# Kernel optimization log

Measured on AMD Instinct MI355X. Metric: run time of the kernel, lower is better.

## Reference

```python
import jax, jax.numpy as jnp
import numpy as np

N_SPK = 2048
M_UTT = 16
D_EMB = 512
EPS = 1e-8  # torch cosine_similarity eps


def setup_inputs() -> dict:
    key = jax.random.key(0)
    k1, = jax.random.split(key, 1)
    speaker_vectors = jax.random.normal(k1, (N_SPK * M_UTT, D_EMB), dtype=jnp.float32)
    return {
        "speaker_vectors": speaker_vectors,
        "w": jnp.float32(10.0),
        "b": jnp.float32(-5.0),
        "speakers": N_SPK,
    }


def _normalize(x):
    # torch.cosine_similarity clamps each norm at eps
    n = jnp.maximum(jnp.linalg.norm(x, axis=-1, keepdims=True), EPS)
    return x / n


def reference(speaker_vectors, w, b, speakers):
    N = speakers
    NM, D = speaker_vectors.shape
    M = NM // N
    v3 = speaker_vectors.reshape(N, M, D)
    ssum = v3.sum(axis=1)                         # [N, D] per-speaker sums
    C = ssum / M                                  # full centroids [N, D]
    C_min = (ssum[:, None, :] - v3) / (M - 1)     # leave-one-out centroids [N, M, D]

    vn = _normalize(speaker_vectors)              # [NM, D]
    # diagonal similarities: cos(C_min[j], v[j]) per utterance j
    S_diag = jnp.sum(_normalize(C_min.reshape(NM, D)) * vn, axis=-1)  # [NM]
    # full similarity matrix via one normalized matmul: [N, NM]
    S_full = _normalize(C) @ vn.T
    # replace each speaker's own block row entries with leave-one-out sims
    col_spk = jnp.arange(NM) // M                 # speaker id of each column
    same = col_spk[None, :] == jnp.arange(N)[:, None]  # [N, NM]
    S = jnp.where(same, S_diag[None, :], S_full)

    # L_j = -(w*S_diag_j + b) + log sum_n exp(w*S[n,j] + b)
    L = -(w * S_diag + b) + jax.nn.logsumexp(w * S + b, axis=0)
    return L.sum()
```

## Files before the change

### kernel.cpp

```cpp
#include <hip/hip_runtime.h>
#include <stdint.h>

#define N_SPK 2048
#define M_UTT 16
#define D_EMB 512
#define NM (N_SPK * M_UTT)
#define FP8_SCALE 16.0f

typedef __attribute__((ext_vector_type(4))) float f32x4;

__device__ __forceinline__ void async_copy16(const void* g, void* l) {
    __builtin_amdgcn_global_load_lds(
        (const __attribute__((address_space(1))) unsigned int*)g,
        (__attribute__((address_space(3))) unsigned int*)l,
        16, 0, 0);
}

__global__ __launch_bounds__(256) void prep_kernel(
    const float* __restrict__ V, const float* __restrict__ wp,
    const float* __restrict__ bp, unsigned char* __restrict__ Cn8,
    unsigned char* __restrict__ vn8, float* __restrict__ dterm,
    float* __restrict__ colsum, float* __restrict__ out)
{
    const int spk = blockIdx.x, t = threadIdx.x;
    const int wave = t >> 6, lane = t & 63;
    const float2* vb = (const float2*)(V + (size_t)spk * (M_UTT * D_EMB));

    __shared__ __align__(16) float red[32][264];
    __shared__ float red2[32];
    __shared__ float invs[M_UTT];
    __shared__ float wred[4];

    if (spk < 128) colsum[spk * 256 + t] = 0.f;
    if (spk == 0 && t == 0) out[0] = 0.f;

    float2 p[M_UTT];
#pragma unroll
    for (int m = 0; m < M_UTT; ++m) p[m] = vb[m * 256 + t];

    float2 ss = make_float2(0.f, 0.f);
#pragma unroll
    for (int m = 0; m < M_UTT; ++m) { ss.x += p[m].x; ss.y += p[m].y; }

    float cnp = ss.x * ss.x + ss.y * ss.y;
#pragma unroll
    for (int off = 32; off > 0; off >>= 1) cnp += __shfl_xor(cnp, off);
    if (lane == 0) wred[wave] = cnp;

#pragma unroll
    for (int m = 0; m < M_UTT; ++m) {
        red[m][t]         = ss.x * p[m].x + ss.y * p[m].y;
        red[m + M_UTT][t] = p[m].x * p[m].x + p[m].y * p[m].y;
    }
    __syncthreads();
    const float cn2 = wred[0] + wred[1] + wred[2] + wred[3];

    {
        const int r = t >> 3, s = t & 7;
        const float4* rp = (const float4*)red;
        float4 a = make_float4(0.f, 0.f, 0.f, 0.f);
#pragma unroll
        for (int k = 0; k < 8; ++k) {
            float4 q = rp[r * 66 + s + 8 * k];
            a.x += q.x; a.y += q.y; a.z += q.z; a.w += q.w;
        }
        float v1 = (a.x + a.y) + (a.z + a.w);
        v1 += __shfl_xor(v1, 1);
        v1 += __shfl_xor(v1, 2);
        v1 += __shfl_xor(v1, 4);
        if (s == 0) red2[r] = v1;
    }
    __syncthreads();

    if (t < M_UTT) {
        const float sv = red2[t], vv = red2[t + M_UTT];
        const float cc = cn2 - 2.f * sv + vv;
        const float cv = sv - vv;
        const float dc = fmaxf(sqrtf(fmaxf(cc, 0.f)) * (1.f / (M_UTT - 1)), 1e-8f) * (M_UTT - 1);
        const float dv = fmaxf(sqrtf(vv), 1e-8f);
        dterm[spk * M_UTT + t] = (*wp) * (cv / (dc * dv)) + (*bp);
        invs[t] = FP8_SCALE / dv;
    }
    __syncthreads();

    const float cs = FP8_SCALE / (M_UTT * fmaxf(sqrtf(cn2) * (1.f / M_UTT), 1e-8f));
    {
        int pk = __builtin_amdgcn_cvt_pk_fp8_f32(ss.x * cs, ss.y * cs, 0, false);
        ((unsigned short*)(Cn8 + (size_t)spk * D_EMB))[t] = (unsigned short)pk;
    }
#pragma unroll
    for (int m = 0; m < M_UTT; ++m) {
        const float iv = invs[m];
        int pk = __builtin_amdgcn_cvt_pk_fp8_f32(p[m].x * iv, p[m].y * iv, 0, false);
        ((unsigned short*)(vn8 + ((size_t)(spk * M_UTT + m)) * D_EMB))[t] = (unsigned short)pk;
    }
}

__global__ __launch_bounds__(256) void gemm_kernel(
    const unsigned char* __restrict__ Cn8, const unsigned char* __restrict__ vn8,
    const float* __restrict__ wp, const float* __restrict__ bp,
    float* __restrict__ colsum)
{
    __shared__ __align__(16) unsigned char As[128 * 64];
    __shared__ __align__(16) unsigned char Bs[128 * 64];
    __shared__ float csum[128];

    const int tid = threadIdx.x;
    const int w = tid >> 6, l = tid & 63;
    const int by = blockIdx.x;
    const int bx = blockIdx.y;
    const float wgt = (*wp) * (1.f / (FP8_SCALE * FP8_SCALE));
    const float bsc = *bp;

    if (tid < 128) csum[tid] = 0.f;

    const int srow = w * 32 + (l >> 2);
    const int sj   = ((l & 3) ^ ((l >> 2) ^ (l >> 4))) & 3;
    const unsigned char* Ab = Cn8 + (size_t)(by * 128 + srow) * D_EMB + sj * 16;
    const unsigned char* Bb = vn8 + (size_t)(bx * 128 + srow) * D_EMB + sj * 16;
    unsigned char* AsW = As + w * 2048;
    unsigned char* BsW = Bs + w * 2048;

    const int wm = w & 1, wn = w >> 1;
    const int l16 = l & 15, q = l >> 4;
    const int sl = (l16 ^ (l16 >> 2)) & 3;
    const int off0 = (((q >> 1)    ) ^ sl) * 16 + (q & 1) * 8;
    const int off1 = (((q >> 1) + 2) ^ sl) * 16 + (q & 1) * 8;
    const unsigned char* Ard = As + (wm * 64 + l16) * 64;
    const unsigned char* Brd = Bs + (wn * 64 + l16) * 64;

    f32x4 acc[4][4];
    const f32x4 z = {0.f, 0.f, 0.f, 0.f};
#pragma unroll
    for (int i = 0; i < 4; ++i)
#pragma unroll
        for (int j = 0; j < 4; ++j) acc[i][j] = z;

    for (int kk = 0; kk < D_EMB; kk += 64) {
        __syncthreads();
        async_copy16(Ab + kk, AsW);
        async_copy16(Ab + 16 * D_EMB + kk, AsW + 1024);
        async_copy16(Bb + kk, BsW);
        async_copy16(Bb + 16 * D_EMB + kk, BsW + 1024);
        __syncthreads();
#pragma unroll
        for (int h = 0; h < 2; ++h) {
            const int off = h ? off1 : off0;
            long af[4], bfr[4];
#pragma unroll
            for (int i = 0; i < 4; ++i) af[i] = *(const long*)(Ard + i * 16 * 64 + off);
#pragma unroll
            for (int j = 0; j < 4; ++j) bfr[j] = *(const long*)(Brd + j * 16 * 64 + off);
#pragma unroll
            for (int i = 0; i < 4; ++i)
#pragma unroll
                for (int j = 0; j < 4; ++j)
                    acc[i][j] = __builtin_amdgcn_mfma_f32_16x16x32_fp8_fp8(
                        af[i], bfr[j], acc[i][j], 0, 0, 0);
        }
    }

    const int rowg0 = by * 128 + wm * 64 + q * 4;
    const int colg0 = bx * 128 + wn * 64 + l16;
#pragma unroll
    for (int j = 0; j < 4; ++j) {
        const int colg = colg0 + j * 16;
        const int cspk = colg >> 4;
        float p = 0.f;
#pragma unroll
        for (int i = 0; i < 4; ++i) {
            const int rowg = rowg0 + i * 16;
#pragma unroll
            for (int r = 0; r < 4; ++r) {
                float e = __expf(wgt * acc[i][j][r] + bsc);
                p += (rowg + r == cspk) ? 0.f : e;
            }
        }
        p += __shfl_xor(p, 16);
        p += __shfl_xor(p, 32);
        if (q == 0) atomicAdd(&csum[wn * 64 + j * 16 + l16], p);
    }
    __syncthreads();
    if (tid < 128) atomicAdd(&colsum[bx * 128 + tid], csum[tid]);
}

__global__ __launch_bounds__(256) void finish_kernel(
    const float* __restrict__ dterm, const float* __restrict__ colsum,
    float* __restrict__ out)
{
    const int idx = blockIdx.x * 256 + threadIdx.x;
    const int stride = gridDim.x * 256;
    float local = 0.f;
    for (int j = idx; j < NM; j += stride) {
        float t = dterm[j];
        local += logf(colsum[j] + __expf(t)) - t;
    }
#pragma unroll
    for (int off = 32; off > 0; off >>= 1) local += __shfl_xor(local, off);
    __shared__ float wr[4];
    const int wave = threadIdx.x >> 6, lane = threadIdx.x & 63;
    if (lane == 0) wr[wave] = local;
    __syncthreads();
    if (threadIdx.x == 0) atomicAdd(out, wr[0] + wr[1] + wr[2] + wr[3]);
}

extern "C" void kernel_launch(void* const* d_in, const int* in_sizes, int n_in,
                              void* d_out, int out_size, void* d_ws, size_t ws_size,
                              hipStream_t stream) {
    const float* V  = (const float*)d_in[0];
    const float* wp = (const float*)d_in[1];
    const float* bp = (const float*)d_in[2];

    char* ws = (char*)d_ws;
    unsigned char* Cn8 = (unsigned char*)ws;
    unsigned char* vn8 = (unsigned char*)(ws + ((size_t)1 << 20));
    float* dterm  = (float*)(ws + ((size_t)17 << 20));
    float* colsum = dterm + NM;
    float* out    = (float*)d_out;

    prep_kernel<<<N_SPK, 256, 0, stream>>>(V, wp, bp, Cn8, vn8, dterm, colsum, out);
    gemm_kernel<<<dim3(N_SPK / 128, NM / 128), 256, 0, stream>>>(Cn8, vn8, wp, bp, colsum);
    finish_kernel<<<64, 256, 0, stream>>>(dterm, colsum, out);
}
```

Before: 153.1 us.

## Use scaled 16x16x128 FP8 MFMA with 128-wide K tiles and fuse finish into GEMM

```diff
diff --git a/kernel.cpp b/kernel.cpp
--- a/kernel.cpp
+++ b/kernel.cpp
@@ -8,6 +8,8 @@
 #define FP8_SCALE 16.0f
 
 typedef __attribute__((ext_vector_type(4))) float f32x4;
+typedef __attribute__((ext_vector_type(4))) int   i32x4;
+typedef __attribute__((ext_vector_type(8))) int   i32x8;
 
 __device__ __forceinline__ void async_copy16(const void* g, void* l) {
     __builtin_amdgcn_global_load_lds(
@@ -16,11 +18,17 @@
         16, 0, 0);
 }
 
+__device__ __forceinline__ i32x8 ld_frag(const unsigned char* base, int s0) {
+    i32x4 lo = *(const i32x4*)(base + s0 * 16);
+    i32x4 hi = *(const i32x4*)(base + (s0 ^ 1) * 16);
+    return __builtin_shufflevector(lo, hi, 0, 1, 2, 3, 4, 5, 6, 7);
+}
+
 __global__ __launch_bounds__(256) void prep_kernel(
     const float* __restrict__ V, const float* __restrict__ wp,
     const float* __restrict__ bp, unsigned char* __restrict__ Cn8,
     unsigned char* __restrict__ vn8, float* __restrict__ dterm,
-    float* __restrict__ colsum, float* __restrict__ out)
+    float* __restrict__ colsum, int* __restrict__ cnt, float* __restrict__ out)
 {
     const int spk = blockIdx.x, t = threadIdx.x;
     const int wave = t >> 6, lane = t & 63;
@@ -32,6 +40,7 @@
     __shared__ float wred[4];
 
     if (spk < 128) colsum[spk * 256 + t] = 0.f;
+    if (spk == 128) cnt[t] = 0;
     if (spk == 0 && t == 0) out[0] = 0.f;
 
     float2 p[M_UTT];
@@ -99,11 +108,14 @@
 __global__ __launch_bounds__(256) void gemm_kernel(
     const unsigned char* __restrict__ Cn8, const unsigned char* __restrict__ vn8,
     const float* __restrict__ wp, const float* __restrict__ bp,
-    float* __restrict__ colsum)
+    float* __restrict__ colsum, const float* __restrict__ dterm,
+    int* __restrict__ cnt, float* __restrict__ out)
 {
-    __shared__ __align__(16) unsigned char As[128 * 64];
-    __shared__ __align__(16) unsigned char Bs[128 * 64];
+    __shared__ __align__(16) unsigned char As[128 * 128];
+    __shared__ __align__(16) unsigned char Bs[128 * 128];
     __shared__ float csum[128];
+    __shared__ float fin[2];
+    __shared__ int lastf;
 
     const int tid = threadIdx.x;
     const int w = tid >> 6, l = tid & 63;
@@ -114,20 +126,18 @@
 
     if (tid < 128) csum[tid] = 0.f;
 
-    const int srow = w * 32 + (l >> 2);
-    const int sj   = ((l & 3) ^ ((l >> 2) ^ (l >> 4))) & 3;
-    const unsigned char* Ab = Cn8 + (size_t)(by * 128 + srow) * D_EMB + sj * 16;
-    const unsigned char* Bb = vn8 + (size_t)(bx * 128 + srow) * D_EMB + sj * 16;
-    unsigned char* AsW = As + w * 2048;
-    unsigned char* BsW = Bs + w * 2048;
+    const int srow = w * 32 + (l >> 3);
+    const int sg   = (l & 7) ^ ((l >> 3) & 7);
+    const unsigned char* Ab = Cn8 + (size_t)(by * 128 + srow) * D_EMB + sg * 16;
+    const unsigned char* Bb = vn8 + (size_t)(bx * 128 + srow) * D_EMB + sg * 16;
+    unsigned char* AsW = As + (w * 32) * 128;
+    unsigned char* BsW = Bs + (w * 32) * 128;
 
     const int wm = w & 1, wn = w >> 1;
     const int l16 = l & 15, q = l >> 4;
-    const int sl = (l16 ^ (l16 >> 2)) & 3;
-    const int off0 = (((q >> 1)    ) ^ sl) * 16 + (q & 1) * 8;
-    const int off1 = (((q >> 1) + 2) ^ sl) * 16 + (q & 1) * 8;
-    const unsigned char* Ard = As + (wm * 64 + l16) * 64;
-    const unsigned char* Brd = Bs + (wn * 64 + l16) * 64;
+    const int s0 = ((l >> 3) & 6) ^ (l & 7);
+    const unsigned char* Ard = As + (wm * 64 + l16) * 128;
+    const unsigned char* Brd = Bs + (wn * 64 + l16) * 128;
 
     f32x4 acc[4][4];
     const f32x4 z = {0.f, 0.f, 0.f, 0.f};
@@ -136,27 +146,24 @@
 #pragma unroll
         for (int j = 0; j < 4; ++j) acc[i][j] = z;
 
-    for (int kk = 0; kk < D_EMB; kk += 64) {
+    for (int kk = 0; kk < D_EMB; kk += 128) {
         __syncthreads();
-        async_copy16(Ab + kk, AsW);
-        async_copy16(Ab + 16 * D_EMB + kk, AsW + 1024);
-        async_copy16(Bb + kk, BsW);
-        async_copy16(Bb + 16 * D_EMB + kk, BsW + 1024);
+#pragma unroll
+        for (int i = 0; i < 4; ++i) {
+            async_copy16(Ab + kk + (size_t)(i * 8) * D_EMB, AsW + i * 1024);
+            async_copy16(Bb + kk + (size_t)(i * 8) * D_EMB, BsW + i * 1024);
+        }
         __syncthreads();
-#pragma unroll
-        for (int h = 0; h < 2; ++h) {
-            const int off = h ? off1 : off0;
-            long af[4], bfr[4];
-#pragma unroll
-            for (int i = 0; i < 4; ++i) af[i] = *(const long*)(Ard + i * 16 * 64 + off);
-#pragma unroll
-            for (int j = 0; j < 4; ++j) bfr[j] = *(const long*)(Brd + j * 16 * 64 + off);
-#pragma unroll
-            for (int i = 0; i < 4; ++i)
-#pragma unroll
-                for (int j = 0; j < 4; ++j)
-                    acc[i][j] = __builtin_amdgcn_mfma_f32_16x16x32_fp8_fp8(
-                        af[i], bfr[j], acc[i][j], 0, 0, 0);
+        i32x8 bfr[4];
+#pragma unroll
+        for (int j = 0; j < 4; ++j) bfr[j] = ld_frag(Brd + j * 2048, s0);
+#pragma unroll
+        for (int i = 0; i < 4; ++i) {
+            i32x8 af = ld_frag(Ard + i * 2048, s0);
+#pragma unroll
+            for (int j = 0; j < 4; ++j)
+                acc[i][j] = __builtin_amdgcn_mfma_scale_f32_16x16x128_f8f6f4(
+                    af, bfr[j], acc[i][j], 0, 0, 0, 0x7F7F7F7F, 0, 0x7F7F7F7F);
         }
     }
 
@@ -182,26 +189,28 @@
     }
     __syncthreads();
     if (tid < 128) atomicAdd(&colsum[bx * 128 + tid], csum[tid]);
-}
-
-__global__ __launch_bounds__(256) void finish_kernel(
-    const float* __restrict__ dterm, const float* __restrict__ colsum,
-    float* __restrict__ out)
-{
-    const int idx = blockIdx.x * 256 + threadIdx.x;
-    const int stride = gridDim.x * 256;
-    float local = 0.f;
-    for (int j = idx; j < NM; j += stride) {
-        float t = dterm[j];
-        local += logf(colsum[j] + __expf(t)) - t;
-    }
-#pragma unroll
-    for (int off = 32; off > 0; off >>= 1) local += __shfl_xor(local, off);
-    __shared__ float wr[4];
-    const int wave = threadIdx.x >> 6, lane = threadIdx.x & 63;
-    if (lane == 0) wr[wave] = local;
-    __syncthreads();
-    if (threadIdx.x == 0) atomicAdd(out, wr[0] + wr[1] + wr[2] + wr[3]);
+    __syncthreads();
+
+    if (tid == 0) {
+        __threadfence();
+        lastf = (atomicAdd(&cnt[bx], 1) == (int)gridDim.x - 1);
+    }
+    __syncthreads();
+    if (lastf) {
+        __threadfence();
+        float loc = 0.f;
+        if (tid < 128) {
+            const int jj = bx * 128 + tid;
+            const float csv = atomicAdd(&colsum[jj], 0.0f);
+            const float dt  = dterm[jj];
+            loc = logf(csv + __expf(dt)) - dt;
+        }
+#pragma unroll
+        for (int off = 32; off > 0; off >>= 1) loc += __shfl_xor(loc, off);
+        if (l == 0 && w < 2) fin[w] = loc;
+        __syncthreads();
+        if (tid == 0) atomicAdd(out, fin[0] + fin[1]);
+    }
 }
 
 extern "C" void kernel_launch(void* const* d_in, const int* in_sizes, int n_in,
@@ -216,9 +225,10 @@
     unsigned char* vn8 = (unsigned char*)(ws + ((size_t)1 << 20));
     float* dterm  = (float*)(ws + ((size_t)17 << 20));
     float* colsum = dterm + NM;
+    int*   cnt    = (int*)(colsum + NM);
     float* out    = (float*)d_out;
 
-    prep_kernel<<<N_SPK, 256, 0, stream>>>(V, wp, bp, Cn8, vn8, dterm, colsum, out);
-    gemm_kernel<<<dim3(N_SPK / 128, NM / 128), 256, 0, stream>>>(Cn8, vn8, wp, bp, colsum);
-    finish_kernel<<<64, 256, 0, stream>>>(dterm, colsum, out);
-}
+    prep_kernel<<<N_SPK, 256, 0, stream>>>(V, wp, bp, Cn8, vn8, dterm, colsum, cnt, out);
+    gemm_kernel<<<dim3(N_SPK / 128, NM / 128), 256, 0, stream>>>(
+        Cn8, vn8, wp, bp, colsum, dterm, cnt, out);
+}
```

Result: slower. 445.1 us (+190.7%).

## Switch GEMM to 16x16x128 scaled FP8 MFMA with 256-byte K tiles

Applied to the files above, without the earlier changes.

```diff
diff --git a/kernel.cpp b/kernel.cpp
--- a/kernel.cpp
+++ b/kernel.cpp
@@ -8,12 +8,20 @@
 #define FP8_SCALE 16.0f
 
 typedef __attribute__((ext_vector_type(4))) float f32x4;
+typedef __attribute__((ext_vector_type(4))) int   i32x4;
+typedef __attribute__((ext_vector_type(8))) int   i32x8;
 
 __device__ __forceinline__ void async_copy16(const void* g, void* l) {
     __builtin_amdgcn_global_load_lds(
         (const __attribute__((address_space(1))) unsigned int*)g,
         (__attribute__((address_space(3))) unsigned int*)l,
         16, 0, 0);
+}
+
+__device__ __forceinline__ i32x8 ld_frag(const unsigned char* base, int s0) {
+    i32x4 lo = *(const i32x4*)(base + s0 * 16);
+    i32x4 hi = *(const i32x4*)(base + (s0 ^ 1) * 16);
+    return __builtin_shufflevector(lo, hi, 0, 1, 2, 3, 4, 5, 6, 7);
 }
 
 __global__ __launch_bounds__(256) void prep_kernel(
@@ -101,8 +109,8 @@
     const float* __restrict__ wp, const float* __restrict__ bp,
     float* __restrict__ colsum)
 {
-    __shared__ __align__(16) unsigned char As[128 * 64];
-    __shared__ __align__(16) unsigned char Bs[128 * 64];
+    __shared__ __align__(16) unsigned char As[128 * 256];
+    __shared__ __align__(16) unsigned char Bs[128 * 256];
     __shared__ float csum[128];
 
     const int tid = threadIdx.x;
@@ -114,20 +122,21 @@
 
     if (tid < 128) csum[tid] = 0.f;
 
-    const int srow = w * 32 + (l >> 2);
-    const int sj   = ((l & 3) ^ ((l >> 2) ^ (l >> 4))) & 3;
-    const unsigned char* Ab = Cn8 + (size_t)(by * 128 + srow) * D_EMB + sj * 16;
-    const unsigned char* Bb = vn8 + (size_t)(bx * 128 + srow) * D_EMB + sj * 16;
-    unsigned char* AsW = As + w * 2048;
-    unsigned char* BsW = Bs + w * 2048;
+    const int r_l = l >> 4, hh = (l >> 3) & 1, sl8 = l & 7;
+    const int g_even = sl8 ^ r_l;
+    const size_t rowoff = (size_t)(w * 32 + r_l) * D_EMB + hh * 128;
+    const unsigned char* Ab0 = Cn8 + (size_t)(by * 128) * D_EMB + rowoff + g_even * 16;
+    const unsigned char* Ab1 = Cn8 + (size_t)(by * 128) * D_EMB + rowoff + (g_even ^ 4) * 16;
+    const unsigned char* Bb0 = vn8 + (size_t)(bx * 128) * D_EMB + rowoff + g_even * 16;
+    const unsigned char* Bb1 = vn8 + (size_t)(bx * 128) * D_EMB + rowoff + (g_even ^ 4) * 16;
+    unsigned char* AsW = As + (w * 32) * 256;
+    unsigned char* BsW = Bs + (w * 32) * 256;
 
     const int wm = w & 1, wn = w >> 1;
     const int l16 = l & 15, q = l >> 4;
-    const int sl = (l16 ^ (l16 >> 2)) & 3;
-    const int off0 = (((q >> 1)    ) ^ sl) * 16 + (q & 1) * 8;
-    const int off1 = (((q >> 1) + 2) ^ sl) * 16 + (q & 1) * 8;
-    const unsigned char* Ard = As + (wm * 64 + l16) * 64;
-    const unsigned char* Brd = Bs + (wn * 64 + l16) * 64;
+    const int s0 = (2 * q) ^ (l & 7);
+    const unsigned char* Ard = As + (wm * 64 + l16) * 256;
+    const unsigned char* Brd = Bs + (wn * 64 + l16) * 256;
 
     f32x4 acc[4][4];
     const f32x4 z = {0.f, 0.f, 0.f, 0.f};
@@ -136,27 +145,31 @@
 #pragma unroll
         for (int j = 0; j < 4; ++j) acc[i][j] = z;
 
-    for (int kk = 0; kk < D_EMB; kk += 64) {
+#pragma unroll
+    for (int kk = 0; kk < D_EMB; kk += 256) {
         __syncthreads();
-        async_copy16(Ab + kk, AsW);
-        async_copy16(Ab + 16 * D_EMB + kk, AsW + 1024);
-        async_copy16(Bb + kk, BsW);
-        async_copy16(Bb + 16 * D_EMB + kk, BsW + 1024);
+#pragma unroll
+        for (int i = 0; i < 8; ++i) {
+            const unsigned char* pa = ((i & 1) ? Ab1 : Ab0) + i * 2048 + kk;
+            const unsigned char* pb = ((i & 1) ? Bb1 : Bb0) + i * 2048 + kk;
+            async_copy16(pa, AsW + i * 1024);
+            async_copy16(pb, BsW + i * 1024);
+        }
         __syncthreads();
 #pragma unroll
-        for (int h = 0; h < 2; ++h) {
-            const int off = h ? off1 : off0;
-            long af[4], bfr[4];
-#pragma unroll
-            for (int i = 0; i < 4; ++i) af[i] = *(const long*)(Ard + i * 16 * 64 + off);
-#pragma unroll
-            for (int j = 0; j < 4; ++j) bfr[j] = *(const long*)(Brd + j * 16 * 64 + off);
-#pragma unroll
-            for (int i = 0; i < 4; ++i)
+        for (int h2 = 0; h2 < 2; ++h2) {
+            const int ho = h2 * 128;
+            i32x8 bfr[4];
+#pragma unroll
+            for (int j = 0; j < 4; ++j) bfr[j] = ld_frag(Brd + j * 4096 + ho, s0);
+#pragma unroll
+            for (int i = 0; i < 4; ++i) {
+                i32x8 af = ld_frag(Ard + i * 4096 + ho, s0);
 #pragma unroll
                 for (int j = 0; j < 4; ++j)
-                    acc[i][j] = __builtin_amdgcn_mfma_f32_16x16x32_fp8_fp8(
-                        af[i], bfr[j], acc[i][j], 0, 0, 0);
+                    acc[i][j] = __builtin_amdgcn_mfma_scale_f32_16x16x128_f8f6f4(
+                        af, bfr[j], acc[i][j], 0, 0, 0, 0x7F7F7F7F, 0, 0x7F7F7F7F);
+            }
         }
     }
 
```

Measured after the change: 149.2 us. 2.6% less time.
